# Kernel optimization log

Hardware: AMD Instinct MI355X
Metric: run time of the kernel (lower is better)

The kernel has to match this reference:

```python
import jax, jax.numpy as jnp
import numpy as np

B_SZ, D_MODEL, L_SEQ = 2, 1024, 2048
D_INNER, D_STATE, DT_RANK, D_CONV = 2 * D_MODEL, 16, 64, 4
EPS = 1e-5


def causal_conv(x, w, b):
    # x: (B, Din, L), w: (Din, 1, K) depthwise, causal pad K-1 on the left
    y = jax.lax.conv_general_dilated(
        x, w, window_strides=(1,), padding=[(D_CONV - 1, 0)],
        dimension_numbers=('NCH', 'OIH', 'NCH'),
        feature_group_count=x.shape[1])
    return y + b[None, :, None]


def selective_scan(u, delta, A, Bm, Cm):
    # u, delta: (B, Din, L); A: (Din, N); Bm, Cm: (B, N, L)
    def step(h, inp):
        dt_t, B_t, C_t, u_t = inp  # (B,Din),(B,N),(B,N),(B,Din)
        h = jnp.exp(dt_t[..., None] * A) * h + (dt_t * u_t)[..., None] * B_t[:, None, :]
        y = jnp.einsum('bdn,bn->bd', h, C_t)
        return h, y

    bsz, din, _ = u.shape
    h0 = jnp.zeros((bsz, din, A.shape[1]), u.dtype)
    inps = (jnp.moveaxis(delta, 2, 0), jnp.moveaxis(Bm, 2, 0),
            jnp.moveaxis(Cm, 2, 0), jnp.moveaxis(u, 2, 0))
    _, ys = jax.lax.scan(step, h0, inps)  # (L, B, Din)
    return jnp.moveaxis(ys, 0, 2)  # (B, Din, L)


def mamba_dir(xz, conv_w, conv_b, xproj_w, dtproj_w, dtproj_b, A_log, Dp):
    # xz: (B, 2*Din, L)
    x, z = xz[:, :D_INNER], xz[:, D_INNER:]
    x = jax.nn.silu(causal_conv(x, conv_w, conv_b))
    x_dbl = jnp.einsum('rd,bdl->brl', xproj_w, x)  # (B, dt_rank+2N, L)
    dt = x_dbl[:, :DT_RANK]
    Bm = x_dbl[:, DT_RANK:DT_RANK + D_STATE]
    Cm = x_dbl[:, DT_RANK + D_STATE:]
    delta = jax.nn.softplus(jnp.einsum('dr,brl->bdl', dtproj_w, dt) + dtproj_b[None, :, None])
    A = -jnp.exp(A_log)
    y = selective_scan(x, delta, A, Bm, Cm) + Dp[None, :, None] * x
    return y * jax.nn.silu(z)


def setup_inputs() -> dict:
    key = jax.random.key(0)
    ks = jax.random.split(key, 20)
    s = 0.02
    A_init = jnp.log(jnp.tile(jnp.arange(1, D_STATE + 1, dtype=jnp.float32)[None, :], (D_INNER, 1)))
    return {
        'hidden_states': jax.random.normal(ks[0], (B_SZ, D_MODEL, L_SEQ), jnp.float32),
        'residual': jax.random.normal(ks[1], (B_SZ, D_MODEL, L_SEQ), jnp.float32),
        'gamma': jnp.ones((D_MODEL,), jnp.float32),
        'beta': jnp.zeros((D_MODEL,), jnp.float32),
        'in_proj_w': jax.random.normal(ks[2], (2 * D_INNER, D_MODEL), jnp.float32) * s,
        'conv_w': jax.random.normal(ks[3], (D_INNER, 1, D_CONV), jnp.float32) * 0.1,
        'conv_b': jnp.zeros((D_INNER,), jnp.float32),
        'xproj_w': jax.random.normal(ks[4], (DT_RANK + 2 * D_STATE, D_INNER), jnp.float32) * s,
        'dtproj_w': jax.random.normal(ks[5], (D_INNER, DT_RANK), jnp.float32) * s,
        'dtproj_b': jax.random.uniform(ks[6], (D_INNER,), jnp.float32, -4.0, -2.0),
        'A_log': A_init,
        'Dp': jnp.ones((D_INNER,), jnp.float32),
        'conv_w_b': jax.random.normal(ks[7], (D_INNER, 1, D_CONV), jnp.float32) * 0.1,
        'conv_b_b': jnp.zeros((D_INNER,), jnp.float32),
        'xproj_w_b': jax.random.normal(ks[8], (DT_RANK + 2 * D_STATE, D_INNER), jnp.float32) * s,
        'dtproj_w_b': jax.random.normal(ks[9], (D_INNER, DT_RANK), jnp.float32) * s,
        'dtproj_b_b': jax.random.uniform(ks[10], (D_INNER,), jnp.float32, -4.0, -2.0),
        'A_b_log': A_init,
        'Dp_b': jnp.ones((D_INNER,), jnp.float32),
        'out_proj_w': jax.random.normal(ks[11], (D_MODEL, D_INNER), jnp.float32) * s,
        'out_proj_b': jnp.zeros((D_MODEL,), jnp.float32),
    }


def reference(hidden_states, residual, gamma, beta, in_proj_w,
              conv_w, conv_b, xproj_w, dtproj_w, dtproj_b, A_log, Dp,
              conv_w_b, conv_b_b, xproj_w_b, dtproj_w_b, dtproj_b_b, A_b_log, Dp_b,
              out_proj_w, out_proj_b):
    h = jnp.transpose(hidden_states, (0, 2, 1))  # (B, L, D)
    r = jnp.transpose(residual, (0, 2, 1)) + h   # residual add (drop_path = Identity)
    # LayerNorm over D
    mu = r.mean(-1, keepdims=True)
    var = ((r - mu) ** 2).mean(-1, keepdims=True)
    hn = (r - mu) * jax.lax.rsqrt(var + EPS) * gamma + beta
    # Mamba bimamba v2
    xz = jnp.einsum('ed,bld->bel', in_proj_w, hn)  # (B, 2*Din, L)
    y_f = mamba_dir(xz, conv_w, conv_b, xproj_w, dtproj_w, dtproj_b, A_log, Dp)
    y_b = mamba_dir(xz[..., ::-1], conv_w_b, conv_b_b, xproj_w_b, dtproj_w_b, dtproj_b_b, A_b_log, Dp_b)
    y = y_f + y_b[..., ::-1]  # (B, Din, L)
    out = jnp.einsum('bdl,ed->ble', y, out_proj_w) + out_proj_b  # (B, L, D)
    return jnp.transpose(out, (0, 2, 1)), jnp.transpose(r, (0, 2, 1))
```

## Files before the change

### kernel.cpp

```cpp
#include <hip/hip_runtime.h>
#include <hip/hip_bf16.h>

typedef __hip_bfloat16 bf16;
typedef __attribute__((ext_vector_type(8))) short short8;
typedef __attribute__((ext_vector_type(4))) float f32x4;

#define L_SEQ 2048
#define D_MODEL 1024
#define D_INNER 2048

static __device__ __forceinline__ float b2f(bf16 v) { return __bfloat162float(v); }

static __device__ __forceinline__ float ldf(const void* p, long i, bool bf) {
  return bf ? __bfloat162float(((const bf16*)p)[i]) : ((const float*)p)[i];
}
static __device__ __forceinline__ void stf(void* p, long i, bool bf, float v) {
  if (bf) ((bf16*)p)[i] = __float2bfloat16(v);
  else    ((float*)p)[i] = v;
}
static __device__ __forceinline__ bool isbf(const unsigned* gb) {
  return gb[0] != 0x3F800000u;
}

__global__ void cast_pad(const void* __restrict__ src, bf16* __restrict__ dst,
                         const unsigned* __restrict__ gb, int n_src, int n_tot) {
  bool bf = isbf(gb);
  int i = blockIdx.x * 256 + threadIdx.x;
  if (i < n_tot) dst[i] = __float2bfloat16(i < n_src ? ldf(src, i, bf) : 0.f);
}

__global__ __launch_bounds__(256)
void ln_stats(const void* __restrict__ hs, const void* __restrict__ res,
              void* __restrict__ dout, float* __restrict__ part,
              const unsigned* __restrict__ gb) {
  bool bf = isbf(gb);
  __shared__ float redS[4][64], redQ[4][64];
  int b = blockIdx.y;
  int l0 = blockIdx.x * 64;
  int dc = blockIdx.z;
  int d0 = dc * 128;
  int t = threadIdx.x;
  int lj = t & 63, g = t >> 6;
  float s = 0.f, sq = 0.f;
#pragma unroll
  for (int r = 0; r < 32; r++) {
    int di = g + 4 * r;
    long gidx = ((long)(b * D_MODEL + d0 + di)) * L_SEQ + l0 + lj;
    float v = ldf(hs, gidx, bf) + ldf(res, gidx, bf);
    stf(dout, 4194304L + gidx, bf, v);
    s += v; sq += v * v;
  }
  redS[g][lj] = s; redQ[g][lj] = sq;
  __syncthreads();
  if (t < 64) {
    float S = redS[0][t] + redS[1][t] + redS[2][t] + redS[3][t];
    float Q = redQ[0][t] + redQ[1][t] + redQ[2][t] + redQ[3][t];
    long pidx = (((long)b * L_SEQ + l0 + t) * 8 + dc) * 2;
    part[pidx] = S; part[pidx + 1] = Q;
  }
}

__global__ __launch_bounds__(256)
void ln_apply(const void* __restrict__ dout, const float* __restrict__ part,
              const void* __restrict__ g, const void* __restrict__ bt,
              bf16* __restrict__ hnb, const unsigned* __restrict__ gb) {
  bool bf = isbf(gb);
  __shared__ float tile[64][65];
  __shared__ float muA[64], rsA[64];
  int b = blockIdx.y;
  int l0 = blockIdx.x * 64;
  int d0 = blockIdx.z * 64;
  int t = threadIdx.x;
  if (t < 64) {
    long base = ((long)b * L_SEQ + l0 + t) * 16;
    float S = 0.f, Q = 0.f;
#pragma unroll
    for (int c = 0; c < 8; c++) { S += part[base + 2 * c]; Q += part[base + 2 * c + 1]; }
    float mu = S * (1.f / 1024.f);
    float var = Q * (1.f / 1024.f) - mu * mu;
    muA[t] = mu; rsA[t] = rsqrtf(var + 1e-5f);
  }
  __syncthreads();
#pragma unroll
  for (int r = 0; r < 16; r++) {
    int idx = t + 256 * r;
    int di = idx >> 6, lj = idx & 63;
    long gidx = ((long)(b * D_MODEL + d0 + di)) * L_SEQ + l0 + lj;
    float v = ldf(dout, 4194304L + gidx, bf);
    v = (v - muA[lj]) * rsA[lj] * ldf(g, d0 + di, bf) + ldf(bt, d0 + di, bf);
    tile[lj][di] = v;
  }
  __syncthreads();
#pragma unroll
  for (int r = 0; r < 16; r++) {
    int idx = t + 256 * r;
    int li = idx >> 6, dj = idx & 63;
    hnb[((long)(b * L_SEQ + l0 + li)) * D_MODEL + d0 + dj] = __float2bfloat16(tile[li][dj]);
  }
}

template <int EPI>
__global__ __launch_bounds__(256)
void mgemm(const bf16* __restrict__ A, const bf16* __restrict__ B,
           const void* __restrict__ bias,
           float* __restrict__ Cf, bf16* __restrict__ Cb, void* __restrict__ Cout,
           const unsigned* __restrict__ gb,
           int M, int N, int K, int lda, int ldb, int ldc,
           long sAb, long sBb, long sCb) {
  bool bf = isbf(gb);
  __shared__ unsigned short As[128][40];
  __shared__ unsigned short Bs[128][40];
  int bz = blockIdx.z;
  const bf16* Ab = A + (long)bz * sAb;
  const bf16* Bp = B + (long)bz * sBb;
  int m0 = blockIdx.y * 128, n0 = blockIdx.x * 128;
  int t = threadIdx.x;
  int lane = t & 63, w = t >> 6;
  int wm = (w >> 1) * 64, wn = (w & 1) * 64;
  int q = lane >> 4, rr = lane & 15;

  f32x4 acc[4][4];
#pragma unroll
  for (int i = 0; i < 4; i++)
#pragma unroll
    for (int j = 0; j < 4; j++) acc[i][j] = (f32x4){0.f, 0.f, 0.f, 0.f};

  for (int k0 = 0; k0 < K; k0 += 32) {
#pragma unroll
    for (int r = 0; r < 2; r++) {
      int idx = t + 256 * r;
      int row = idx >> 2, seg = idx & 3;
      int m = m0 + row;
      uint4 v = make_uint4(0u, 0u, 0u, 0u);
      if (m < M) v = *(const uint4*)(Ab + (long)m * lda + k0 + seg * 8);
      *(uint4*)&As[row][seg * 8] = v;
    }
#pragma unroll
    for (int r = 0; r < 2; r++) {
      int idx = t + 256 * r;
      int row = idx >> 2, seg = idx & 3;
      uint4 v = *(const uint4*)(Bp + (long)(n0 + row) * ldb + k0 + seg * 8);
      *(uint4*)&Bs[row][seg * 8] = v;
    }
    __syncthreads();
    short8 af[4], bv[4];
#pragma unroll
    for (int mi = 0; mi < 4; mi++) af[mi] = *(const short8*)&As[wm + mi * 16 + rr][q * 8];
#pragma unroll
    for (int ni = 0; ni < 4; ni++) bv[ni] = *(const short8*)&Bs[wn + ni * 16 + rr][q * 8];
#pragma unroll
    for (int mi = 0; mi < 4; mi++)
#pragma unroll
      for (int ni = 0; ni < 4; ni++)
        acc[mi][ni] = __builtin_amdgcn_mfma_f32_16x16x32_bf16(af[mi], bv[ni], acc[mi][ni], 0, 0, 0);
    __syncthreads();
  }

#pragma unroll
  for (int mi = 0; mi < 4; mi++) {
#pragma unroll
    for (int ni = 0; ni < 4; ni++) {
      f32x4 a = acc[mi][ni];
#pragma unroll
      for (int reg = 0; reg < 4; reg++) {
        int m = m0 + wm + mi * 16 + q * 4 + reg;
        int n = n0 + wn + ni * 16 + rr;
        if (m < M && n < N) {
          float v = a[reg];
          if (EPI == 2) {
            v += ldf(bias, m, bf);
            stf(Cout, (long)bz * sCb + (long)m * ldc + n, bf, v);
          } else if (EPI == 3) {
            Cb[(long)bz * sCb + (long)m * ldc + n] = __float2bfloat16(v);
          } else if (EPI == 4) {
            v += ldf(bias, n, bf);
            v = (v > 0.f) ? (v + log1pf(expf(-v))) : log1pf(expf(v));
            Cf[(long)bz * sCb + (long)m * ldc + n] = v;
          } else if (EPI == 5) {
            Cf[(long)bz * sCb + (long)m * ldc + n] = v;
            if (n < 64) Cb[(long)bz * (long)M * 64 + (long)m * 64 + n] = __float2bfloat16(v);
          }
        }
      }
    }
  }
}

__global__ void conv_t_kernel(const bf16* __restrict__ xzb,
                              const void* __restrict__ wF, const void* __restrict__ bF,
                              const void* __restrict__ wB, const void* __restrict__ bB,
                              bf16* __restrict__ xcT, const unsigned* __restrict__ gb) {
  bool bf = isbf(gb);
  __shared__ float xs[64][68];
  __shared__ float ys[64][65];
  int zz = blockIdx.z;
  int dir = zz >> 1, b = zz & 1;
  int t0 = blockIdx.x * 64, d0 = blockIdx.y * 64;
  int t = threadIdx.x;
  const void* wsel = dir ? wB : wF;
  const void* bsel = dir ? bB : bF;
  for (int i = t; i < 64 * 67; i += 256) {
    int di = i / 67, j = i % 67;
    int tt = t0 - 3 + j;
    float v = 0.f;
    if (tt >= 0) {
      int l = dir ? (2047 - tt) : tt;
      v = b2f(xzb[((long)b * 4096 + d0 + di) * 2048 + l]);
    }
    xs[di][j] = v;
  }
  __syncthreads();
  {
    int di = t >> 2, jq = (t & 3) * 16;
    int d = d0 + di;
    float w0 = ldf(wsel, d * 4 + 0, bf), w1 = ldf(wsel, d * 4 + 1, bf);
    float w2 = ldf(wsel, d * 4 + 2, bf), w3 = ldf(wsel, d * 4 + 3, bf);
    float bi = ldf(bsel, d, bf);
#pragma unroll
    for (int jj = 0; jj < 16; jj++) {
      int j = jq + jj;
      float acc = bi + w0 * xs[di][j] + w1 * xs[di][j + 1] + w2 * xs[di][j + 2] + w3 * xs[di][j + 3];
      ys[j][di] = acc / (1.f + __expf(-acc));
    }
  }
  __syncthreads();
  for (int r = 0; r < 16; r++) {
    int idx = t + 256 * r;
    int li = idx >> 6, dj = idx & 63;
    xcT[((long)zz * 2048 + t0 + li) * 2048 + d0 + dj] = __float2bfloat16(ys[li][dj]);
  }
}

__global__ __launch_bounds__(256)
void scan_p1(const float* __restrict__ deltaT, const bf16* __restrict__ xcT,
             const float* __restrict__ xdblT,
             const void* __restrict__ AlogF, const void* __restrict__ AlogB,
             const unsigned* __restrict__ gb, float* __restrict__ trans) {
  bool bf = isbf(gb);
  int zz = blockIdx.z;
  int dir = zz >> 1;
  int d = blockIdx.y * 256 + threadIdx.x;
  int c = blockIdx.x, l0 = c * 64;
  const void* Alog = dir ? AlogB : AlogF;
  float Av[16], h[16], S[16];
#pragma unroll
  for (int n = 0; n < 16; n++) {
    Av[n] = -__expf(ldf(Alog, (long)d * 16 + n, bf) * 1.44269504f) ;
  }
#pragma unroll
  for (int n = 0; n < 16; n++) { h[n] = 0.f; S[n] = 1.f; }
  const float* dT = deltaT + ((long)zz * 2048 + l0) * 2048 + d;
  const bf16* uT = xcT + ((long)zz * 2048 + l0) * 2048 + d;
  const float* BC = xdblT + ((long)zz * 2048 + l0) * 96;
  for (int j = 0; j < 64; j++) {
    float dt = dT[(long)j * 2048];
    float u = b2f(uT[(long)j * 2048]);
    float du = dt * u;
    const float* bc = BC + j * 96;
#pragma unroll
    for (int qq = 0; qq < 4; qq++) {
      float4 Bq = *(const float4*)(bc + 64 + qq * 4);
#pragma unroll
      for (int k = 0; k < 4; k++) {
        int n = qq * 4 + k;
        float e = __expf(dt * Av[n] * 1.44269504f);
        S[n] *= e;
        float bb = (k == 0) ? Bq.x : (k == 1) ? Bq.y : (k == 2) ? Bq.z : Bq.w;
        h[n] = e * h[n] + du * bb;
      }
    }
  }
  float* tp = trans + (((long)zz * 32 + c) * 32) * 2048 + d;
#pragma unroll
  for (int n = 0; n < 16; n++) {
    tp[(long)n * 2048] = S[n];
    tp[(long)(16 + n) * 2048] = h[n];
  }
}

__global__ void scan_chain(float* __restrict__ trans) {
  int idx = blockIdx.x * 256 + threadIdx.x;
  int d = idx & 2047;
  int n = (idx >> 11) & 15;
  int zz = idx >> 15;
  float h = 0.f;
  for (int c = 0; c < 32; c++) {
    long base = (((long)zz * 32 + c) * 32) * 2048 + d;
    float S = trans[base + (long)n * 2048];
    float hl = trans[base + (long)(16 + n) * 2048];
    trans[base + (long)n * 2048] = h;
    h = S * h + hl;
  }
}

__global__ __launch_bounds__(256)
void scan_p2(float* deltaT, const bf16* __restrict__ xcT,
             const float* __restrict__ xdblT,
             const void* __restrict__ AlogF, const void* __restrict__ AlogB,
             const void* __restrict__ DpF, const void* __restrict__ DpB,
             const unsigned* __restrict__ gb, const float* __restrict__ trans) {
  bool bf = isbf(gb);
  int zz = blockIdx.z;
  int dir = zz >> 1;
  int d = blockIdx.y * 256 + threadIdx.x;
  int c = blockIdx.x, l0 = c * 64;
  const void* Alog = dir ? AlogB : AlogF;
  const void* Dpp  = dir ? DpB : DpF;
  float Av[16], h[16];
#pragma unroll
  for (int n = 0; n < 16; n++)
    Av[n] = -__expf(ldf(Alog, (long)d * 16 + n, bf) * 1.44269504f);
  const float* hp = trans + (((long)zz * 32 + c) * 32) * 2048 + d;
#pragma unroll
  for (int n = 0; n < 16; n++) h[n] = hp[(long)n * 2048];
  float Dval = ldf(Dpp, d, bf);
  float* dT = deltaT + ((long)zz * 2048 + l0) * 2048 + d;
  const bf16* uT = xcT + ((long)zz * 2048 + l0) * 2048 + d;
  const float* BC = xdblT + ((long)zz * 2048 + l0) * 96;
  for (int j = 0; j < 64; j++) {
    float dt = dT[(long)j * 2048];
    float u = b2f(uT[(long)j * 2048]);
    float du = dt * u;
    const float* bc = BC + j * 96;
    float y = Dval * u;
#pragma unroll
    for (int qq = 0; qq < 4; qq++) {
      float4 Bq = *(const float4*)(bc + 64 + qq * 4);
      float4 Cq = *(const float4*)(bc + 80 + qq * 4);
#pragma unroll
      for (int k = 0; k < 4; k++) {
        int n = qq * 4 + k;
        float e = __expf(dt * Av[n] * 1.44269504f);
        float bb = (k == 0) ? Bq.x : (k == 1) ? Bq.y : (k == 2) ? Bq.z : Bq.w;
        float cc = (k == 0) ? Cq.x : (k == 1) ? Cq.y : (k == 2) ? Cq.z : Cq.w;
        h[n] = e * h[n] + du * bb;
        y += h[n] * cc;
      }
    }
    dT[(long)j * 2048] = y;
  }
}

__global__ void combine_t(const float* __restrict__ yT, const bf16* __restrict__ xzb,
                          bf16* __restrict__ ygT) {
  __shared__ float zs[64][65];
  int b = blockIdx.z;
  int l0 = blockIdx.x * 64, d0 = blockIdx.y * 64;
  int t = threadIdx.x;
#pragma unroll
  for (int r = 0; r < 16; r++) {
    int idx = t + 256 * r;
    int di = idx >> 6, lj = idx & 63;
    zs[di][lj] = b2f(xzb[((long)b * 4096 + 2048 + d0 + di) * 2048 + l0 + lj]);
  }
  __syncthreads();
#pragma unroll
  for (int r = 0; r < 16; r++) {
    int idx = t + 256 * r;
    int li = idx >> 6, dj = idx & 63;
    int l = l0 + li;
    float yf = yT[((long)(0 * 2 + b) * 2048 + l) * 2048 + d0 + dj];
    float yb = yT[((long)(2 + b) * 2048 + (2047 - l)) * 2048 + d0 + dj];
    float z = zs[dj][li];
    float sz = z / (1.f + __expf(-z));
    ygT[((long)b * 2048 + l) * 2048 + d0 + dj] = __float2bfloat16((yf + yb) * sz);
  }
}

extern "C" void kernel_launch(void* const* d_in, const int* in_sizes, int n_in,
                              void* d_out, int out_size, void* d_ws, size_t ws_size,
                              hipStream_t stream) {
  const void* hs     = d_in[0];
  const void* res    = d_in[1];
  const void* gamma  = d_in[2];
  const void* beta   = d_in[3];
  const void* inw    = d_in[4];
  const void* convw  = d_in[5];
  const void* convb  = d_in[6];
  const void* xprojw = d_in[7];
  const void* dtw    = d_in[8];
  const void* dtb    = d_in[9];
  const void* Alog   = d_in[10];
  const void* Dpv    = d_in[11];
  const void* convwb = d_in[12];
  const void* convbb = d_in[13];
  const void* xprojwb= d_in[14];
  const void* dtwb   = d_in[15];
  const void* dtbb   = d_in[16];
  const void* Ablog  = d_in[17];
  const void* Dpb    = d_in[18];
  const void* outw   = d_in[19];
  const void* outb   = d_in[20];
  const unsigned* gb = (const unsigned*)gamma;

  float* ws = (float*)d_ws;
  bf16*  hnb    = (bf16*)(ws);
  bf16*  xzb    = (bf16*)(ws + 2097152L);
  bf16*  xcT    = (bf16*)(ws + 10485760L);
  float* xdblT  = ws + 18874368L;
  bf16*  xdbl_dt= (bf16*)(ws + 19660800L);
  float* deltaT = ws + 19922944L;
  float* trans  = ws + 36700160L;
  bf16*  ygT    = (bf16*)trans;
  bf16*  wInw   = (bf16*)(ws + 45088768L);
  bf16*  wOut   = (bf16*)(ws + 47185920L);
  bf16*  wXpad  = (bf16*)(ws + 48234496L);
  bf16*  wDt    = (bf16*)(ws + 48496640L);
  float* lnpart = ws + 48627712L;

  cast_pad<<<dim3(16384), 256, 0, stream>>>(inw,  wInw, gb, 4194304, 4194304);
  cast_pad<<<dim3(8192),  256, 0, stream>>>(outw, wOut, gb, 2097152, 2097152);
  cast_pad<<<dim3(1024),  256, 0, stream>>>(xprojw,  wXpad,           gb, 196608, 262144);
  cast_pad<<<dim3(1024),  256, 0, stream>>>(xprojwb, wXpad + 262144,  gb, 196608, 262144);
  cast_pad<<<dim3(512),   256, 0, stream>>>(dtw,     wDt,             gb, 131072, 131072);
  cast_pad<<<dim3(512),   256, 0, stream>>>(dtwb,    wDt + 131072,    gb, 131072, 131072);

  ln_stats<<<dim3(32, 2, 8), 256, 0, stream>>>(hs, res, d_out, lnpart, gb);
  ln_apply<<<dim3(32, 2, 16), 256, 0, stream>>>(d_out, lnpart, gamma, beta, hnb, gb);

  mgemm<3><<<dim3(16, 32, 2), 256, 0, stream>>>(
      wInw, hnb, nullptr, nullptr, xzb, nullptr, gb,
      4096, 2048, 1024, 1024, 1024, 2048, 0L, 2048L * 1024L, 4096L * 2048L);

  conv_t_kernel<<<dim3(32, 32, 4), 256, 0, stream>>>(xzb, convw, convb, convwb, convbb, xcT, gb);

  mgemm<5><<<dim3(1, 32, 2), 256, 0, stream>>>(
      xcT, wXpad, nullptr, xdblT, xdbl_dt, nullptr, gb,
      4096, 96, 2048, 2048, 2048, 96, 4096L * 2048L, 128L * 2048L, 4096L * 96L);

  mgemm<4><<<dim3(16, 32, 1), 256, 0, stream>>>(
      xdbl_dt, wDt, dtb, deltaT, nullptr, nullptr, gb,
      4096, 2048, 64, 64, 64, 2048, 0L, 0L, 0L);
  mgemm<4><<<dim3(16, 32, 1), 256, 0, stream>>>(
      xdbl_dt + 4096L * 64L, wDt + 131072, dtbb, deltaT + 4096L * 2048L,
      nullptr, nullptr, gb,
      4096, 2048, 64, 64, 64, 2048, 0L, 0L, 0L);

  scan_p1<<<dim3(32, 8, 4), 256, 0, stream>>>(deltaT, xcT, xdblT, Alog, Ablog, gb, trans);
  scan_chain<<<dim3(512), 256, 0, stream>>>(trans);
  scan_p2<<<dim3(32, 8, 4), 256, 0, stream>>>(deltaT, xcT, xdblT, Alog, Ablog, Dpv, Dpb, gb, trans);

  combine_t<<<dim3(32, 32, 2), 256, 0, stream>>>(deltaT, xzb, ygT);

  mgemm<2><<<dim3(16, 8, 2), 256, 0, stream>>>(
      wOut, ygT, outb, nullptr, nullptr, d_out, gb,
      1024, 2048, 2048, 2048, 2048, 2048, 0L, 2048L * 2048L, 1024L * 2048L);
}
```

Baseline: 679.2 us.

## Specialize scan for integer A, store delta/y in bf16, merge launches

New measurement: 827.8 us. 1.22x slower.

```diff
diff --git a/kernel.cpp b/kernel.cpp
--- a/kernel.cpp
+++ b/kernel.cpp
@@ -22,11 +22,32 @@
   return gb[0] != 0x3F800000u;
 }
 
-__global__ void cast_pad(const void* __restrict__ src, bf16* __restrict__ dst,
-                         const unsigned* __restrict__ gb, int n_src, int n_tot) {
-  bool bf = isbf(gb);
-  int i = blockIdx.x * 256 + threadIdx.x;
-  if (i < n_tot) dst[i] = __float2bfloat16(i < n_src ? ldf(src, i, bf) : 0.f);
+__global__ void cast_all(const void* __restrict__ s0, const void* __restrict__ s1,
+                         const void* __restrict__ s2, const void* __restrict__ s3,
+                         const void* __restrict__ s4, const void* __restrict__ s5,
+                         bf16* __restrict__ d0, bf16* __restrict__ d1, bf16* __restrict__ d2,
+                         bf16* __restrict__ d3, bf16* __restrict__ d4, bf16* __restrict__ d5,
+                         const unsigned* __restrict__ gb) {
+  bool bf = isbf(gb);
+  long i = (long)blockIdx.x * 256 + threadIdx.x;
+  if (i < 4194304L) {
+    d0[i] = __float2bfloat16(ldf(s0, i, bf));
+  } else if (i < 6291456L) {
+    long j = i - 4194304L;
+    d1[j] = __float2bfloat16(ldf(s1, j, bf));
+  } else if (i < 6553600L) {
+    long j = i - 6291456L;
+    d2[j] = __float2bfloat16(j < 196608L ? ldf(s2, j, bf) : 0.f);
+  } else if (i < 6815744L) {
+    long j = i - 6553600L;
+    d3[j] = __float2bfloat16(j < 196608L ? ldf(s3, j, bf) : 0.f);
+  } else if (i < 6946816L) {
+    long j = i - 6815744L;
+    d4[j] = __float2bfloat16(ldf(s4, j, bf));
+  } else if (i < 7077888L) {
+    long j = i - 6946816L;
+    d5[j] = __float2bfloat16(ldf(s5, j, bf));
+  }
 }
 
 __global__ __launch_bounds__(256)
@@ -102,7 +123,7 @@
 template <int EPI>
 __global__ __launch_bounds__(256)
 void mgemm(const bf16* __restrict__ A, const bf16* __restrict__ B,
-           const void* __restrict__ bias,
+           const void* __restrict__ bias, const void* __restrict__ bias2,
            float* __restrict__ Cf, bf16* __restrict__ Cb, void* __restrict__ Cout,
            const unsigned* __restrict__ gb,
            int M, int N, int K, int lda, int ldb, int ldc,
@@ -173,9 +194,10 @@
           } else if (EPI == 3) {
             Cb[(long)bz * sCb + (long)m * ldc + n] = __float2bfloat16(v);
           } else if (EPI == 4) {
-            v += ldf(bias, n, bf);
+            const void* bp = bz ? bias2 : bias;
+            v += ldf(bp, n, bf);
             v = (v > 0.f) ? (v + log1pf(expf(-v))) : log1pf(expf(v));
-            Cf[(long)bz * sCb + (long)m * ldc + n] = v;
+            Cb[(long)bz * sCb + (long)m * ldc + n] = __float2bfloat16(v);
           } else if (EPI == 5) {
             Cf[(long)bz * sCb + (long)m * ldc + n] = v;
             if (n < 64) Cb[(long)bz * (long)M * 64 + (long)m * 64 + n] = __float2bfloat16(v);
@@ -232,50 +254,77 @@
 }
 
 __global__ __launch_bounds__(256)
-void scan_p1(const float* __restrict__ deltaT, const bf16* __restrict__ xcT,
+void scan_p1(const bf16* __restrict__ deltaT, const bf16* __restrict__ xcT,
              const float* __restrict__ xdblT,
              const void* __restrict__ AlogF, const void* __restrict__ AlogB,
              const unsigned* __restrict__ gb, float* __restrict__ trans) {
   bool bf = isbf(gb);
-  int zz = blockIdx.z;
-  int dir = zz >> 1;
+  int zz = blockIdx.z, dir = zz >> 1;
   int d = blockIdx.y * 256 + threadIdx.x;
   int c = blockIdx.x, l0 = c * 64;
   const void* Alog = dir ? AlogB : AlogF;
-  float Av[16], h[16], S[16];
+  float Av[16];
+  bool fast = true;
 #pragma unroll
   for (int n = 0; n < 16; n++) {
-    Av[n] = -__expf(ldf(Alog, (long)d * 16 + n, bf) * 1.44269504f) ;
-  }
-#pragma unroll
-  for (int n = 0; n < 16; n++) { h[n] = 0.f; S[n] = 1.f; }
-  const float* dT = deltaT + ((long)zz * 2048 + l0) * 2048 + d;
+    Av[n] = -__expf(ldf(Alog, (long)d * 16 + n, bf) * 1.44269504f);
+    fast = fast && (fabsf(Av[n] + (float)(n + 1)) < 3e-3f * (float)(n + 1));
+  }
+  float h[16];
+#pragma unroll
+  for (int n = 0; n < 16; n++) h[n] = 0.f;
+  float dtsum = 0.f;
+  const bf16* dT = deltaT + ((long)zz * 2048 + l0) * 2048 + d;
   const bf16* uT = xcT + ((long)zz * 2048 + l0) * 2048 + d;
   const float* BC = xdblT + ((long)zz * 2048 + l0) * 96;
-  for (int j = 0; j < 64; j++) {
-    float dt = dT[(long)j * 2048];
-    float u = b2f(uT[(long)j * 2048]);
-    float du = dt * u;
-    const float* bc = BC + j * 96;
-#pragma unroll
-    for (int qq = 0; qq < 4; qq++) {
-      float4 Bq = *(const float4*)(bc + 64 + qq * 4);
-#pragma unroll
-      for (int k = 0; k < 4; k++) {
-        int n = qq * 4 + k;
+  if (fast) {
+    for (int j = 0; j < 64; j++) {
+      float dt = b2f(dT[(long)j * 2048]);
+      float du = dt * b2f(uT[(long)j * 2048]);
+      dtsum += dt;
+      const float* bc = BC + j * 96;
+      float Bv[16];
+#pragma unroll
+      for (int qq = 0; qq < 4; qq++) {
+        float4 q4 = *(const float4*)(bc + 64 + qq * 4);
+        Bv[qq * 4] = q4.x; Bv[qq * 4 + 1] = q4.y; Bv[qq * 4 + 2] = q4.z; Bv[qq * 4 + 3] = q4.w;
+      }
+      float E = __expf(-dt * 1.44269504f);
+      float e = 1.f;
+#pragma unroll
+      for (int n = 0; n < 16; n++) { e *= E; h[n] = e * h[n] + du * Bv[n]; }
+    }
+  } else {
+    for (int j = 0; j < 64; j++) {
+      float dt = b2f(dT[(long)j * 2048]);
+      float du = dt * b2f(uT[(long)j * 2048]);
+      dtsum += dt;
+      const float* bc = BC + j * 96;
+      float Bv[16];
+#pragma unroll
+      for (int qq = 0; qq < 4; qq++) {
+        float4 q4 = *(const float4*)(bc + 64 + qq * 4);
+        Bv[qq * 4] = q4.x; Bv[qq * 4 + 1] = q4.y; Bv[qq * 4 + 2] = q4.z; Bv[qq * 4 + 3] = q4.w;
+      }
+#pragma unroll
+      for (int n = 0; n < 16; n++) {
         float e = __expf(dt * Av[n] * 1.44269504f);
-        S[n] *= e;
-        float bb = (k == 0) ? Bq.x : (k == 1) ? Bq.y : (k == 2) ? Bq.z : Bq.w;
-        h[n] = e * h[n] + du * bb;
+        h[n] = e * h[n] + du * Bv[n];
       }
     }
   }
   float* tp = trans + (((long)zz * 32 + c) * 32) * 2048 + d;
-#pragma unroll
-  for (int n = 0; n < 16; n++) {
-    tp[(long)n * 2048] = S[n];
-    tp[(long)(16 + n) * 2048] = h[n];
-  }
+  if (fast) {
+    float Et = __expf(-dtsum * 1.44269504f);
+    float s = 1.f;
+#pragma unroll
+    for (int n = 0; n < 16; n++) { s *= Et; tp[(long)n * 2048] = s; }
+  } else {
+#pragma unroll
+    for (int n = 0; n < 16; n++) tp[(long)n * 2048] = __expf(Av[n] * dtsum * 1.44269504f);
+  }
+#pragma unroll
+  for (int n = 0; n < 16; n++) tp[(long)(16 + n) * 2048] = h[n];
 }
 
 __global__ void scan_chain(float* __restrict__ trans) {
@@ -294,54 +343,84 @@
 }
 
 __global__ __launch_bounds__(256)
-void scan_p2(float* deltaT, const bf16* __restrict__ xcT,
+void scan_p2(bf16* deltaT, const bf16* __restrict__ xcT,
              const float* __restrict__ xdblT,
              const void* __restrict__ AlogF, const void* __restrict__ AlogB,
              const void* __restrict__ DpF, const void* __restrict__ DpB,
              const unsigned* __restrict__ gb, const float* __restrict__ trans) {
   bool bf = isbf(gb);
-  int zz = blockIdx.z;
-  int dir = zz >> 1;
+  int zz = blockIdx.z, dir = zz >> 1;
   int d = blockIdx.y * 256 + threadIdx.x;
   int c = blockIdx.x, l0 = c * 64;
   const void* Alog = dir ? AlogB : AlogF;
   const void* Dpp  = dir ? DpB : DpF;
-  float Av[16], h[16];
-#pragma unroll
-  for (int n = 0; n < 16; n++)
+  float Av[16];
+  bool fast = true;
+#pragma unroll
+  for (int n = 0; n < 16; n++) {
     Av[n] = -__expf(ldf(Alog, (long)d * 16 + n, bf) * 1.44269504f);
+    fast = fast && (fabsf(Av[n] + (float)(n + 1)) < 3e-3f * (float)(n + 1));
+  }
   const float* hp = trans + (((long)zz * 32 + c) * 32) * 2048 + d;
+  float h[16];
 #pragma unroll
   for (int n = 0; n < 16; n++) h[n] = hp[(long)n * 2048];
   float Dval = ldf(Dpp, d, bf);
-  float* dT = deltaT + ((long)zz * 2048 + l0) * 2048 + d;
+  bf16* dT = deltaT + ((long)zz * 2048 + l0) * 2048 + d;
   const bf16* uT = xcT + ((long)zz * 2048 + l0) * 2048 + d;
   const float* BC = xdblT + ((long)zz * 2048 + l0) * 96;
-  for (int j = 0; j < 64; j++) {
-    float dt = dT[(long)j * 2048];
-    float u = b2f(uT[(long)j * 2048]);
-    float du = dt * u;
-    const float* bc = BC + j * 96;
-    float y = Dval * u;
-#pragma unroll
-    for (int qq = 0; qq < 4; qq++) {
-      float4 Bq = *(const float4*)(bc + 64 + qq * 4);
-      float4 Cq = *(const float4*)(bc + 80 + qq * 4);
-#pragma unroll
-      for (int k = 0; k < 4; k++) {
-        int n = qq * 4 + k;
+  if (fast) {
+    for (int j = 0; j < 64; j++) {
+      float dt = b2f(dT[(long)j * 2048]);
+      float u = b2f(uT[(long)j * 2048]);
+      float du = dt * u;
+      const float* bc = BC + j * 96;
+      float Bv[16], Cv[16];
+#pragma unroll
+      for (int qq = 0; qq < 4; qq++) {
+        float4 q4 = *(const float4*)(bc + 64 + qq * 4);
+        Bv[qq * 4] = q4.x; Bv[qq * 4 + 1] = q4.y; Bv[qq * 4 + 2] = q4.z; Bv[qq * 4 + 3] = q4.w;
+        float4 c4 = *(const float4*)(bc + 80 + qq * 4);
+        Cv[qq * 4] = c4.x; Cv[qq * 4 + 1] = c4.y; Cv[qq * 4 + 2] = c4.z; Cv[qq * 4 + 3] = c4.w;
+      }
+      float E = __expf(-dt * 1.44269504f);
+      float e = 1.f;
+      float y = Dval * u;
+#pragma unroll
+      for (int n = 0; n < 16; n++) {
+        e *= E;
+        h[n] = e * h[n] + du * Bv[n];
+        y += h[n] * Cv[n];
+      }
+      dT[(long)j * 2048] = __float2bfloat16(y);
+    }
+  } else {
+    for (int j = 0; j < 64; j++) {
+      float dt = b2f(dT[(long)j * 2048]);
+      float u = b2f(uT[(long)j * 2048]);
+      float du = dt * u;
+      const float* bc = BC + j * 96;
+      float Bv[16], Cv[16];
+#pragma unroll
+      for (int qq = 0; qq < 4; qq++) {
+        float4 q4 = *(const float4*)(bc + 64 + qq * 4);
+        Bv[qq * 4] = q4.x; Bv[qq * 4 + 1] = q4.y; Bv[qq * 4 + 2] = q4.z; Bv[qq * 4 + 3] = q4.w;
+        float4 c4 = *(const float4*)(bc + 80 + qq * 4);
+        Cv[qq * 4] = c4.x; Cv[qq * 4 + 1] = c4.y; Cv[qq * 4 + 2] = c4.z; Cv[qq * 4 + 3] = c4.w;
+      }
+      float y = Dval * u;
+#pragma unroll
+      for (int n = 0; n < 16; n++) {
         float e = __expf(dt * Av[n] * 1.44269504f);
-        float bb = (k == 0) ? Bq.x : (k == 1) ? Bq.y : (k == 2) ? Bq.z : Bq.w;
-        float cc = (k == 0) ? Cq.x : (k == 1) ? Cq.y : (k == 2) ? Cq.z : Cq.w;
-        h[n] = e * h[n] + du * bb;
-        y += h[n] * cc;
-      }
-    }
-    dT[(long)j * 2048] = y;
-  }
-}
-
-__global__ void combine_t(const float* __restrict__ yT, const bf16* __restrict__ xzb,
+        h[n] = e * h[n] + du * Bv[n];
+        y += h[n] * Cv[n];
+      }
+      dT[(long)j * 2048] = __float2bfloat16(y);
+    }
+  }
+}
+
+__global__ void combine_t(const bf16* __restrict__ yT, const bf16* __restrict__ xzb,
                           bf16* __restrict__ ygT) {
   __shared__ float zs[64][65];
   int b = blockIdx.z;
@@ -359,8 +438,8 @@
     int idx = t + 256 * r;
     int li = idx >> 6, dj = idx & 63;
     int l = l0 + li;
-    float yf = yT[((long)(0 * 2 + b) * 2048 + l) * 2048 + d0 + dj];
-    float yb = yT[((long)(2 + b) * 2048 + (2047 - l)) * 2048 + d0 + dj];
+    float yf = b2f(yT[((long)b * 2048 + l) * 2048 + d0 + dj]);
+    float yb = b2f(yT[((long)(2 + b) * 2048 + (2047 - l)) * 2048 + d0 + dj]);
     float z = zs[dj][li];
     float sz = z / (1.f + __expf(-z));
     ygT[((long)b * 2048 + l) * 2048 + d0 + dj] = __float2bfloat16((yf + yb) * sz);
@@ -399,42 +478,35 @@
   bf16*  xcT    = (bf16*)(ws + 10485760L);
   float* xdblT  = ws + 18874368L;
   bf16*  xdbl_dt= (bf16*)(ws + 19660800L);
-  float* deltaT = ws + 19922944L;
-  float* trans  = ws + 36700160L;
+  bf16*  deltaT = (bf16*)(ws + 19922944L);
+  float* trans  = ws + 28311552L;
   bf16*  ygT    = (bf16*)trans;
-  bf16*  wInw   = (bf16*)(ws + 45088768L);
-  bf16*  wOut   = (bf16*)(ws + 47185920L);
-  bf16*  wXpad  = (bf16*)(ws + 48234496L);
-  bf16*  wDt    = (bf16*)(ws + 48496640L);
-  float* lnpart = ws + 48627712L;
-
-  cast_pad<<<dim3(16384), 256, 0, stream>>>(inw,  wInw, gb, 4194304, 4194304);
-  cast_pad<<<dim3(8192),  256, 0, stream>>>(outw, wOut, gb, 2097152, 2097152);
-  cast_pad<<<dim3(1024),  256, 0, stream>>>(xprojw,  wXpad,           gb, 196608, 262144);
-  cast_pad<<<dim3(1024),  256, 0, stream>>>(xprojwb, wXpad + 262144,  gb, 196608, 262144);
-  cast_pad<<<dim3(512),   256, 0, stream>>>(dtw,     wDt,             gb, 131072, 131072);
-  cast_pad<<<dim3(512),   256, 0, stream>>>(dtwb,    wDt + 131072,    gb, 131072, 131072);
+  bf16*  wInw   = (bf16*)(ws + 36700160L);
+  bf16*  wOut   = (bf16*)(ws + 38797312L);
+  bf16*  wXpad  = (bf16*)(ws + 39845888L);
+  bf16*  wDt    = (bf16*)(ws + 40108032L);
+  float* lnpart = ws + 40239104L;
+
+  cast_all<<<dim3(27648), 256, 0, stream>>>(
+      inw, outw, xprojw, xprojwb, dtw, dtwb,
+      wInw, wOut, wXpad, wXpad + 262144, wDt, wDt + 131072, gb);
 
   ln_stats<<<dim3(32, 2, 8), 256, 0, stream>>>(hs, res, d_out, lnpart, gb);
   ln_apply<<<dim3(32, 2, 16), 256, 0, stream>>>(d_out, lnpart, gamma, beta, hnb, gb);
 
   mgemm<3><<<dim3(16, 32, 2), 256, 0, stream>>>(
-      wInw, hnb, nullptr, nullptr, xzb, nullptr, gb,
+      wInw, hnb, nullptr, nullptr, nullptr, xzb, nullptr, gb,
       4096, 2048, 1024, 1024, 1024, 2048, 0L, 2048L * 1024L, 4096L * 2048L);
 
   conv_t_kernel<<<dim3(32, 32, 4), 256, 0, stream>>>(xzb, convw, convb, convwb, convbb, xcT, gb);
 
   mgemm<5><<<dim3(1, 32, 2), 256, 0, stream>>>(
-      xcT, wXpad, nullptr, xdblT, xdbl_dt, nullptr, gb,
+      xcT, wXpad, nullptr, nullptr, xdblT, xdbl_dt, nullptr, gb,
       4096, 96, 2048, 2048, 2048, 96, 4096L * 2048L, 128L * 2048L, 4096L * 96L);
 
-  mgemm<4><<<dim3(16, 32, 1), 256, 0, stream>>>(
-      xdbl_dt, wDt, dtb, deltaT, nullptr, nullptr, gb,
-      4096, 2048, 64, 64, 64, 2048, 0L, 0L, 0L);
-  mgemm<4><<<dim3(16, 32, 1), 256, 0, stream>>>(
-      xdbl_dt + 4096L * 64L, wDt + 131072, dtbb, deltaT + 4096L * 2048L,
-      nullptr, nullptr, gb,
-      4096, 2048, 64, 64, 64, 2048, 0L, 0L, 0L);
+  mgemm<4><<<dim3(16, 32, 2), 256, 0, stream>>>(
+      xdbl_dt, wDt, dtb, dtbb, nullptr, deltaT, nullptr, gb,
+      4096, 2048, 64, 64, 64, 2048, 4096L * 64L, 131072L, 4096L * 2048L);
 
   scan_p1<<<dim3(32, 8, 4), 256, 0, stream>>>(deltaT, xcT, xdblT, Alog, Ablog, gb, trans);
   scan_chain<<<dim3(512), 256, 0, stream>>>(trans);
@@ -443,6 +515,6 @@
   combine_t<<<dim3(32, 32, 2), 256, 0, stream>>>(deltaT, xzb, ygT);
 
   mgemm<2><<<dim3(16, 8, 2), 256, 0, stream>>>(
-      wOut, ygT, outb, nullptr, nullptr, d_out, gb,
+      wOut, ygT, outb, nullptr, nullptr, nullptr, d_out, gb,
       1024, 2048, 2048, 2048, 2048, 2048, 0L, 2048L * 2048L, 1024L * 2048L);
 }
```
